# Optimization experiments

Measured on AMD Instinct MI355X. Metric: run time of the kernel, lower is better.

The kernel has to match this reference:

```python
import jax, jax.numpy as jnp
import numpy as np

B, T, D, H = 2, 2048, 2048, 16
HD = D // H
EPS = 1e-8
NEG = -1e9


def setup_inputs() -> dict:
    key = jax.random.key(0)
    ks = jax.random.split(key, 6)
    x = jax.random.normal(ks[0], (B, T, D), dtype=jnp.float32)
    # additive causal mask, broadcast over [B, H, T, T]
    causal = jnp.tril(jnp.ones((T, T), dtype=bool))
    attn_mask = jnp.where(causal, 0.0, NEG).astype(jnp.float32)[None, None]
    s = 1.0 / np.sqrt(D)
    w_norm = jnp.ones((D,), dtype=jnp.float32)
    wq = jax.random.normal(ks[1], (D, D), dtype=jnp.float32) * s
    wk = jax.random.normal(ks[2], (D, D), dtype=jnp.float32) * s
    wv = jax.random.normal(ks[3], (D, D), dtype=jnp.float32) * s
    wo = jax.random.normal(ks[4], (D, D), dtype=jnp.float32) * s
    return {"x": x, "attn_mask": attn_mask, "w_norm": w_norm,
            "wq": wq, "wk": wk, "wv": wv, "wo": wo}


def _rmsnorm(x, w):
    # norm = ||x||_2 * D^-0.5 ; out = w * x / (norm + eps)  (eps outside, as in source)
    norm = jnp.sqrt(jnp.sum(x * x, axis=-1, keepdims=True)) * (x.shape[-1] ** -0.5)
    return w * x / (norm + EPS)


def reference(x, attn_mask, w_norm, wq, wk, wv, wo):
    b, t, d = x.shape
    xn = _rmsnorm(x, w_norm)
    # Linear (no bias): y = x @ W^T ; split into heads -> [B, H, T, HD]
    def proj(w):
        return jnp.einsum('btd,ed->bte', xn, w).reshape(b, t, H, HD).transpose(0, 2, 1, 3)
    q, k, v = proj(wq), proj(wk), proj(wv)
    scale = HD ** -0.5
    w_scores = jnp.einsum('bhqd,bhkd->bhqk', q, k) * scale + attn_mask
    p = jax.nn.softmax(w_scores, axis=-1)
    out = jnp.einsum('bhqk,bhkd->bhqd', p, v)
    out = out.transpose(0, 2, 1, 3).reshape(b, t, d)
    return jnp.einsum('btd,ed->bte', out, wo)
```

## Files before the change

### kernel.cpp

```cpp
#include <hip/hip_runtime.h>
#include <stdint.h>

#define TT 2048
#define DD 2048
#define NHH 16
#define HDD 128
#define BTT 4096

typedef __attribute__((ext_vector_type(8))) short bf16x8;
typedef __attribute__((ext_vector_type(4))) float f32x4;

__device__ __forceinline__ unsigned short f2bf(float f) {
    union { float f; uint32_t u; } v; v.f = f;
    uint32_t u = v.u;
    u += 0x7fffu + ((u >> 16) & 1u);
    return (unsigned short)(u >> 16);
}

__device__ __forceinline__ void gld16(const unsigned short* g, unsigned short* l) {
    __builtin_amdgcn_global_load_lds(
        (const __attribute__((address_space(1))) unsigned int*)g,
        (__attribute__((address_space(3))) unsigned int*)l, 16, 0, 0);
}

__global__ __launch_bounds__(256) void convert_w(const float* __restrict__ wq,
                                                 const float* __restrict__ wk,
                                                 const float* __restrict__ wv,
                                                 const float* __restrict__ wo,
                                                 unsigned short* __restrict__ out) {
    size_t gid = (size_t)blockIdx.x * 256 + threadIdx.x;
    size_t base = gid * 8;
    int which = (int)(base >> 22);
    const float* src = which == 0 ? wq : which == 1 ? wk : which == 2 ? wv : wo;
    size_t off = base & 4194303u;
    float4 a = ((const float4*)(src + off))[0];
    float4 b = ((const float4*)(src + off))[1];
    union { unsigned short us[8]; uint4 v; } pk;
    pk.us[0] = f2bf(a.x); pk.us[1] = f2bf(a.y); pk.us[2] = f2bf(a.z); pk.us[3] = f2bf(a.w);
    pk.us[4] = f2bf(b.x); pk.us[5] = f2bf(b.y); pk.us[6] = f2bf(b.z); pk.us[7] = f2bf(b.w);
    *(uint4*)(out + base) = pk.v;
}

__global__ __launch_bounds__(256) void rmsnorm_k(const float* __restrict__ x,
                                                 const float* __restrict__ w,
                                                 unsigned short* __restrict__ xn) {
    const int row = blockIdx.x;
    const int tid = threadIdx.x;
    const float* xr = x + (size_t)row * DD;
    float4 a = ((const float4*)xr)[tid * 2];
    float4 b = ((const float4*)xr)[tid * 2 + 1];
    float ss = a.x*a.x + a.y*a.y + a.z*a.z + a.w*a.w
             + b.x*b.x + b.y*b.y + b.z*b.z + b.w*b.w;
    #pragma unroll
    for (int m = 1; m < 64; m <<= 1) ss += __shfl_xor(ss, m, 64);
    __shared__ float wss[4];
    if ((tid & 63) == 0) wss[tid >> 6] = ss;
    __syncthreads();
    float total = wss[0] + wss[1] + wss[2] + wss[3];
    float norm = sqrtf(total) * 0.022097086912079612f;
    float inv = 1.0f / (norm + 1e-8f);
    float4 wa = ((const float4*)w)[tid * 2];
    float4 wb = ((const float4*)w)[tid * 2 + 1];
    union { unsigned short us[8]; uint4 v; } pk;
    pk.us[0] = f2bf(wa.x * a.x * inv); pk.us[1] = f2bf(wa.y * a.y * inv);
    pk.us[2] = f2bf(wa.z * a.z * inv); pk.us[3] = f2bf(wa.w * a.w * inv);
    pk.us[4] = f2bf(wb.x * b.x * inv); pk.us[5] = f2bf(wb.y * b.y * inv);
    pk.us[6] = f2bf(wb.z * b.z * inv); pk.us[7] = f2bf(wb.w * b.w * inv);
    ((uint4*)(xn + (size_t)row * DD))[tid] = pk.v;
}

__device__ __forceinline__ void gemm_core(const unsigned short* __restrict__ Ag0,
                                          const unsigned short* __restrict__ Bg0,
                                          unsigned short* As, unsigned short* Bs,
                                          int tid, f32x4 acc[4][4]) {
    const int w = tid >> 6, lane = tid & 63;
    const int l15 = lane & 15, lq = lane >> 4;
    const int wr = (w >> 1) * 64, wc = (w & 1) * 64;
    const unsigned short* ag = Ag0 + (size_t)(w * 16 + (lane >> 2)) * DD + (lane & 3) * 8;
    const unsigned short* bg = Bg0 + (size_t)(w * 16 + (lane >> 2)) * DD + (lane & 3) * 8;
    unsigned short* al = As + w * 512;
    unsigned short* bl = Bs + w * 512;
    for (int k0 = 0; k0 < DD; k0 += 32) {
        __syncthreads();
        gld16(ag + k0, al);
        gld16(ag + k0 + (size_t)64 * DD, al + 64 * 32);
        gld16(bg + k0, bl);
        gld16(bg + k0 + (size_t)64 * DD, bl + 64 * 32);
        __syncthreads();
        bf16x8 af[4], bfr[4];
        #pragma unroll
        for (int i = 0; i < 4; i++)
            af[i] = *(const bf16x8*)(As + (wr + i * 16 + l15) * 32 + lq * 8);
        #pragma unroll
        for (int j = 0; j < 4; j++)
            bfr[j] = *(const bf16x8*)(Bs + (wc + j * 16 + l15) * 32 + lq * 8);
        #pragma unroll
        for (int i = 0; i < 4; i++)
            #pragma unroll
            for (int j = 0; j < 4; j++)
                acc[i][j] = __builtin_amdgcn_mfma_f32_16x16x32_bf16(af[i], bfr[j], acc[i][j], 0, 0, 0);
    }
}

__global__ __launch_bounds__(256) void gemm_qkv(const unsigned short* __restrict__ A,
                                                const unsigned short* __restrict__ W3,
                                                unsigned short* __restrict__ O3) {
    __shared__ __align__(16) unsigned short As[128 * 32];
    __shared__ __align__(16) unsigned short Bs[128 * 32];
    const int tid = threadIdx.x;
    const int wave = tid >> 6, lane = tid & 63;
    const int l15 = lane & 15, lq = lane >> 4;
    const int by = blockIdx.y;
    const int which = by >> 4;
    const unsigned short* Bw = W3 + (size_t)which * DD * DD;
    unsigned short* C = O3 + (size_t)which * BTT * DD;
    const int m0 = blockIdx.x * 128, n0 = (by & 15) * 128;
    const int wr = (wave >> 1) * 64, wc = (wave & 1) * 64;
    const f32x4 zf = {0.f, 0.f, 0.f, 0.f};
    f32x4 acc[4][4];
    #pragma unroll
    for (int i = 0; i < 4; i++)
        #pragma unroll
        for (int j = 0; j < 4; j++) acc[i][j] = zf;
    gemm_core(A + (size_t)m0 * DD, Bw + (size_t)n0 * DD, As, Bs, tid, acc);
    #pragma unroll
    for (int i = 0; i < 4; i++) {
        const int row = m0 + wr + i * 16 + lq * 4;
        #pragma unroll
        for (int j = 0; j < 4; j++) {
            const int col = n0 + wc + j * 16 + l15;
            #pragma unroll
            for (int r = 0; r < 4; r++)
                C[(size_t)(row + r) * DD + col] = f2bf(acc[i][j][r]);
        }
    }
}

__global__ __launch_bounds__(256) void gemm_out(const unsigned short* __restrict__ A,
                                                const unsigned short* __restrict__ Bw,
                                                float* __restrict__ C) {
    __shared__ __align__(16) unsigned short As[128 * 32];
    __shared__ __align__(16) unsigned short Bs[128 * 32];
    const int tid = threadIdx.x;
    const int wave = tid >> 6, lane = tid & 63;
    const int l15 = lane & 15, lq = lane >> 4;
    const int m0 = blockIdx.x * 128, n0 = blockIdx.y * 128;
    const int wr = (wave >> 1) * 64, wc = (wave & 1) * 64;
    const f32x4 zf = {0.f, 0.f, 0.f, 0.f};
    f32x4 acc[4][4];
    #pragma unroll
    for (int i = 0; i < 4; i++)
        #pragma unroll
        for (int j = 0; j < 4; j++) acc[i][j] = zf;
    gemm_core(A + (size_t)m0 * DD, Bw + (size_t)n0 * DD, As, Bs, tid, acc);
    #pragma unroll
    for (int i = 0; i < 4; i++) {
        const int row = m0 + wr + i * 16 + lq * 4;
        #pragma unroll
        for (int j = 0; j < 4; j++) {
            const int col = n0 + wc + j * 16 + l15;
            #pragma unroll
            for (int r = 0; r < 4; r++)
                C[(size_t)(row + r) * DD + col] = acc[i][j][r];
        }
    }
}

__global__ __launch_bounds__(256) void attn_fused(const unsigned short* __restrict__ q,
                                                  const unsigned short* __restrict__ k,
                                                  const unsigned short* __restrict__ v,
                                                  unsigned short* __restrict__ o) {
    constexpr int LKK = 136;
    constexpr int LPP = 72;
    __shared__ __align__(16) unsigned short Ks[64 * LKK];
    __shared__ __align__(16) unsigned short Vts[128 * 64];
    __shared__ __align__(16) unsigned short Ps[4 * 16 * LPP];
    const int h = blockIdx.y, b = blockIdx.z;
    const int tid = threadIdx.x, wave = tid >> 6, lane = tid & 63;
    const int l15 = lane & 15, lq = lane >> 4;
    const size_t rowbase = (size_t)b * TT;
    const int hcol = h * HDD;
    const float scale = 0.08838834764831845f;
    unsigned short* Pw = Ps + wave * 16 * LPP;
    const f32x4 zf = {0.f, 0.f, 0.f, 0.f};

    for (int half = 0; half < 2; half++) {
        const int qj = (half == 0) ? blockIdx.x : 31 - blockIdx.x;
        const int qt0 = qj * 64;
        bf16x8 aq[4];
        {
            const unsigned short* qrp = q + (rowbase + qt0 + wave * 16 + l15) * DD + hcol;
            #pragma unroll
            for (int kk = 0; kk < 4; kk++)
                aq[kk] = *(const bf16x8*)(qrp + kk * 32 + lq * 8);
        }
        f32x4 acc_o[8];
        #pragma unroll
        for (int jh = 0; jh < 8; jh++) acc_o[jh] = zf;
        float m_i[4], l_i[4];
        #pragma unroll
        for (int r = 0; r < 4; r++) { m_i[r] = -1e30f; l_i[r] = 0.f; }
        const int qp0 = qt0 + wave * 16 + lq * 4;
        const int nkt = qj + 1;
        for (int kt = 0; kt < nkt; kt++) {
            __syncthreads();
            {
                const unsigned short* kg = k + (rowbase + kt * 64) * DD + hcol;
                const unsigned short* vg = v + (rowbase + kt * 64) * DD + hcol;
                #pragma unroll
                for (int it = 0; it < 4; it++) {
                    const int idx = it * 2048 + tid * 8;
                    const int rr = idx >> 7, c = idx & 127;
                    *(uint4*)(&Ks[rr * LKK + c]) = *(const uint4*)(kg + (size_t)rr * DD + c);
                    uint4 dv = *(const uint4*)(vg + (size_t)rr * DD + c);
                    const unsigned short* ds = (const unsigned short*)&dv;
                    const int rs = rr ^ (((c >> 3) & 7) << 3);
                    #pragma unroll
                    for (int jj = 0; jj < 8; jj++)
                        Vts[(c + jj) * 64 + rs] = ds[jj];
                }
            }
            __syncthreads();
            f32x4 accs[4];
            #pragma unroll
            for (int j = 0; j < 4; j++) accs[j] = zf;
            #pragma unroll
            for (int j = 0; j < 4; j++)
                #pragma unroll
                for (int kk = 0; kk < 4; kk++) {
                    bf16x8 bk = *(const bf16x8*)(&Ks[(j * 16 + l15) * LKK + kk * 32 + lq * 8]);
                    accs[j] = __builtin_amdgcn_mfma_f32_16x16x32_bf16(aq[kk], bk, accs[j], 0, 0, 0);
                }
            const int kbase = kt * 64;
            float rowmax[4] = {-1e30f, -1e30f, -1e30f, -1e30f};
            #pragma unroll
            for (int j = 0; j < 4; j++) {
                const int kp = kbase + j * 16 + l15;
                #pragma unroll
                for (int r = 0; r < 4; r++) {
                    float s = accs[j][r] * scale;
                    s = (kp > qp0 + r) ? -1e30f : s;
                    accs[j][r] = s;
                    rowmax[r] = fmaxf(rowmax[r], s);
                }
            }
            #pragma unroll
            for (int r = 0; r < 4; r++) {
                float mx = rowmax[r];
                mx = fmaxf(mx, __shfl_xor(mx, 1, 64));
                mx = fmaxf(mx, __shfl_xor(mx, 2, 64));
                mx = fmaxf(mx, __shfl_xor(mx, 4, 64));
                mx = fmaxf(mx, __shfl_xor(mx, 8, 64));
                float m_new = fmaxf(m_i[r], mx);
                float al = __expf(m_i[r] - m_new);
                m_i[r] = m_new;
                l_i[r] *= al;
                #pragma unroll
                for (int jh = 0; jh < 8; jh++) acc_o[jh][r] *= al;
            }
            float rowsum[4] = {0.f, 0.f, 0.f, 0.f};
            #pragma unroll
            for (int j = 0; j < 4; j++)
                #pragma unroll
                for (int r = 0; r < 4; r++) {
                    float p = __expf(accs[j][r] - m_i[r]);
                    rowsum[r] += p;
                    Pw[(lq * 4 + r) * LPP + j * 16 + l15] = f2bf(p);
                }
            #pragma unroll
            for (int r = 0; r < 4; r++) {
                float s = rowsum[r];
                s += __shfl_xor(s, 1, 64);
                s += __shfl_xor(s, 2, 64);
                s += __shfl_xor(s, 4, 64);
                s += __shfl_xor(s, 8, 64);
                l_i[r] += s;
            }
            bf16x8 ap[2];
            #pragma unroll
            for (int kk = 0; kk < 2; kk++)
                ap[kk] = *(const bf16x8*)(&Pw[l15 * LPP + kk * 32 + lq * 8]);
            #pragma unroll
            for (int jh = 0; jh < 8; jh++) {
                const int hd = jh * 16 + l15;
                const int swz = ((hd >> 3) & 7) << 3;
                #pragma unroll
                for (int kk = 0; kk < 2; kk++) {
                    bf16x8 bv = *(const bf16x8*)(&Vts[hd * 64 + ((kk * 32 + lq * 8) ^ swz)]);
                    acc_o[jh] = __builtin_amdgcn_mfma_f32_16x16x32_bf16(ap[kk], bv, acc_o[jh], 0, 0, 0);
                }
            }
        }
        #pragma unroll
        for (int jh = 0; jh < 8; jh++) {
            const int col = hcol + jh * 16 + l15;
            #pragma unroll
            for (int r = 0; r < 4; r++)
                o[(rowbase + qp0 + r) * DD + col] = f2bf(acc_o[jh][r] * (1.0f / l_i[r]));
        }
    }
}

extern "C" void kernel_launch(void* const* d_in, const int* in_sizes, int n_in,
                              void* d_out, int out_size, void* d_ws, size_t ws_size,
                              hipStream_t stream) {
    const float* x      = (const float*)d_in[0];
    const float* w_norm = (const float*)d_in[2];
    const float* wq     = (const float*)d_in[3];
    const float* wk     = (const float*)d_in[4];
    const float* wv     = (const float*)d_in[5];
    const float* wo     = (const float*)d_in[6];

    unsigned short* wbf = (unsigned short*)d_ws;
    unsigned short* xn  = wbf + (size_t)4 * DD * DD;
    unsigned short* qb  = xn + (size_t)BTT * DD;
    unsigned short* kb  = qb + (size_t)BTT * DD;
    unsigned short* vb  = kb + (size_t)BTT * DD;
    unsigned short* ab  = vb + (size_t)BTT * DD;

    convert_w<<<8192, 256, 0, stream>>>(wq, wk, wv, wo, wbf);
    rmsnorm_k<<<BTT, 256, 0, stream>>>(x, w_norm, xn);
    dim3 gqkv(32, 48);
    gemm_qkv<<<gqkv, 256, 0, stream>>>(xn, wbf, qb);
    dim3 gattn(16, NHH, 2);
    attn_fused<<<gattn, 256, 0, stream>>>(qb, kb, vb, ab);
    dim3 gout(32, 16);
    gemm_out<<<gout, 256, 0, stream>>>(ab, wbf + (size_t)3 * DD * DD, (float*)d_out);
}
```

Measured before the change: 482.6 us.

## Double-buffer K/V tiles in attention with register prefetch and MFMA priority

The attention kernel now keeps two LDS buffers for the K and transposed-V tiles. It loads the next tile's K/V into registers before computing on the current tile, then writes them to the other buffer afterwards, which removes one barrier per iteration and hides global load latency behind the MFMA work. It also raises wave priority around the MFMA sections with s_setprio. In exchange, LDS use roughly doubles and register pressure grows, which could lower occupancy.

```diff
diff --git a/kernel.cpp b/kernel.cpp
--- a/kernel.cpp
+++ b/kernel.cpp
@@ -172,8 +172,8 @@
                                                   unsigned short* __restrict__ o) {
     constexpr int LKK = 136;
     constexpr int LPP = 72;
-    __shared__ __align__(16) unsigned short Ks[64 * LKK];
-    __shared__ __align__(16) unsigned short Vts[128 * 64];
+    __shared__ __align__(16) unsigned short Ks[2][64 * LKK];
+    __shared__ __align__(16) unsigned short Vts[2][128 * 64];
     __shared__ __align__(16) unsigned short Ps[4 * 16 * LPP];
     const int h = blockIdx.y, b = blockIdx.z;
     const int tid = threadIdx.x, wave = tid >> 6, lane = tid & 63;
@@ -184,6 +184,16 @@
     unsigned short* Pw = Ps + wave * 16 * LPP;
     const f32x4 zf = {0.f, 0.f, 0.f, 0.f};
 
+    uint4 kr0, kr1, kr2, kr3, vr0, vr1, vr2, vr3;
+    const int sidx = tid * 8;
+    const int srr = sidx >> 7;
+    const int sc  = sidx & 127;
+    const int swz = ((sc >> 3) & 7) << 3;
+    const int srs0 = (srr +  0) ^ swz;
+    const int srs1 = (srr + 16) ^ swz;
+    const int srs2 = (srr + 32) ^ swz;
+    const int srs3 = (srr + 48) ^ swz;
+
     for (int half = 0; half < 2; half++) {
         const int qj = (half == 0) ? blockIdx.x : 31 - blockIdx.x;
         const int qt0 = qj * 64;
@@ -202,35 +212,69 @@
         for (int r = 0; r < 4; r++) { m_i[r] = -1e30f; l_i[r] = 0.f; }
         const int qp0 = qt0 + wave * 16 + lq * 4;
         const int nkt = qj + 1;
+
+        __syncthreads();
+        {
+            const unsigned short* kg = k + (rowbase + 0) * DD + hcol;
+            const unsigned short* vg = v + (rowbase + 0) * DD + hcol;
+            kr0 = *(const uint4*)(kg + (size_t)(srr +  0) * DD + sc);
+            kr1 = *(const uint4*)(kg + (size_t)(srr + 16) * DD + sc);
+            kr2 = *(const uint4*)(kg + (size_t)(srr + 32) * DD + sc);
+            kr3 = *(const uint4*)(kg + (size_t)(srr + 48) * DD + sc);
+            vr0 = *(const uint4*)(vg + (size_t)(srr +  0) * DD + sc);
+            vr1 = *(const uint4*)(vg + (size_t)(srr + 16) * DD + sc);
+            vr2 = *(const uint4*)(vg + (size_t)(srr + 32) * DD + sc);
+            vr3 = *(const uint4*)(vg + (size_t)(srr + 48) * DD + sc);
+        }
+        {
+            unsigned short* ksb = &Ks[0][0];
+            unsigned short* vtb = &Vts[0][0];
+            *(uint4*)(ksb + (srr +  0) * LKK + sc) = kr0;
+            *(uint4*)(ksb + (srr + 16) * LKK + sc) = kr1;
+            *(uint4*)(ksb + (srr + 32) * LKK + sc) = kr2;
+            *(uint4*)(ksb + (srr + 48) * LKK + sc) = kr3;
+            const unsigned short* d0 = (const unsigned short*)&vr0;
+            const unsigned short* d1 = (const unsigned short*)&vr1;
+            const unsigned short* d2 = (const unsigned short*)&vr2;
+            const unsigned short* d3 = (const unsigned short*)&vr3;
+            #pragma unroll
+            for (int jj = 0; jj < 8; jj++) {
+                vtb[(sc + jj) * 64 + srs0] = d0[jj];
+                vtb[(sc + jj) * 64 + srs1] = d1[jj];
+                vtb[(sc + jj) * 64 + srs2] = d2[jj];
+                vtb[(sc + jj) * 64 + srs3] = d3[jj];
+            }
+        }
+
         for (int kt = 0; kt < nkt; kt++) {
+            const int cur = kt & 1;
+            if (kt + 1 < nkt) {
+                const unsigned short* kg = k + (rowbase + (kt + 1) * 64) * DD + hcol;
+                const unsigned short* vg = v + (rowbase + (kt + 1) * 64) * DD + hcol;
+                kr0 = *(const uint4*)(kg + (size_t)(srr +  0) * DD + sc);
+                kr1 = *(const uint4*)(kg + (size_t)(srr + 16) * DD + sc);
+                kr2 = *(const uint4*)(kg + (size_t)(srr + 32) * DD + sc);
+                kr3 = *(const uint4*)(kg + (size_t)(srr + 48) * DD + sc);
+                vr0 = *(const uint4*)(vg + (size_t)(srr +  0) * DD + sc);
+                vr1 = *(const uint4*)(vg + (size_t)(srr + 16) * DD + sc);
+                vr2 = *(const uint4*)(vg + (size_t)(srr + 32) * DD + sc);
+                vr3 = *(const uint4*)(vg + (size_t)(srr + 48) * DD + sc);
+            }
             __syncthreads();
-            {
-                const unsigned short* kg = k + (rowbase + kt * 64) * DD + hcol;
-                const unsigned short* vg = v + (rowbase + kt * 64) * DD + hcol;
-                #pragma unroll
-                for (int it = 0; it < 4; it++) {
-                    const int idx = it * 2048 + tid * 8;
-                    const int rr = idx >> 7, c = idx & 127;
-                    *(uint4*)(&Ks[rr * LKK + c]) = *(const uint4*)(kg + (size_t)rr * DD + c);
-                    uint4 dv = *(const uint4*)(vg + (size_t)rr * DD + c);
-                    const unsigned short* ds = (const unsigned short*)&dv;
-                    const int rs = rr ^ (((c >> 3) & 7) << 3);
-                    #pragma unroll
-                    for (int jj = 0; jj < 8; jj++)
-                        Vts[(c + jj) * 64 + rs] = ds[jj];
-                }
-            }
-            __syncthreads();
+            const unsigned short* ksc = &Ks[cur][0];
+            const unsigned short* vtc = &Vts[cur][0];
             f32x4 accs[4];
             #pragma unroll
             for (int j = 0; j < 4; j++) accs[j] = zf;
+            __builtin_amdgcn_s_setprio(1);
             #pragma unroll
             for (int j = 0; j < 4; j++)
                 #pragma unroll
                 for (int kk = 0; kk < 4; kk++) {
-                    bf16x8 bk = *(const bf16x8*)(&Ks[(j * 16 + l15) * LKK + kk * 32 + lq * 8]);
+                    bf16x8 bk = *(const bf16x8*)(&ksc[(j * 16 + l15) * LKK + kk * 32 + lq * 8]);
                     accs[j] = __builtin_amdgcn_mfma_f32_16x16x32_bf16(aq[kk], bk, accs[j], 0, 0, 0);
                 }
+            __builtin_amdgcn_s_setprio(0);
             const int kbase = kt * 64;
             float rowmax[4] = {-1e30f, -1e30f, -1e30f, -1e30f};
             #pragma unroll
@@ -280,14 +324,35 @@
             #pragma unroll
             for (int kk = 0; kk < 2; kk++)
                 ap[kk] = *(const bf16x8*)(&Pw[l15 * LPP + kk * 32 + lq * 8]);
+            __builtin_amdgcn_s_setprio(1);
             #pragma unroll
             for (int jh = 0; jh < 8; jh++) {
                 const int hd = jh * 16 + l15;
-                const int swz = ((hd >> 3) & 7) << 3;
+                const int vswz = ((hd >> 3) & 7) << 3;
                 #pragma unroll
                 for (int kk = 0; kk < 2; kk++) {
-                    bf16x8 bv = *(const bf16x8*)(&Vts[hd * 64 + ((kk * 32 + lq * 8) ^ swz)]);
+                    bf16x8 bv = *(const bf16x8*)(&vtc[hd * 64 + ((kk * 32 + lq * 8) ^ vswz)]);
                     acc_o[jh] = __builtin_amdgcn_mfma_f32_16x16x32_bf16(ap[kk], bv, acc_o[jh], 0, 0, 0);
+                }
+            }
+            __builtin_amdgcn_s_setprio(0);
+            if (kt + 1 < nkt) {
+                unsigned short* ksb = &Ks[cur ^ 1][0];
+                unsigned short* vtb = &Vts[cur ^ 1][0];
+                *(uint4*)(ksb + (srr +  0) * LKK + sc) = kr0;
+                *(uint4*)(ksb + (srr + 16) * LKK + sc) = kr1;
+                *(uint4*)(ksb + (srr + 32) * LKK + sc) = kr2;
+                *(uint4*)(ksb + (srr + 48) * LKK + sc) = kr3;
+                const unsigned short* d0 = (const unsigned short*)&vr0;
+                const unsigned short* d1 = (const unsigned short*)&vr1;
+                const unsigned short* d2 = (const unsigned short*)&vr2;
+                const unsigned short* d3 = (const unsigned short*)&vr3;
+                #pragma unroll
+                for (int jj = 0; jj < 8; jj++) {
+                    vtb[(sc + jj) * 64 + srs0] = d0[jj];
+                    vtb[(sc + jj) * 64 + srs1] = d1[jj];
+                    vtb[(sc + jj) * 64 + srs2] = d2[jj];
+                    vtb[(sc + jj) * 64 + srs3] = d3[jj];
                 }
             }
         }
```

Result: slower. 501.4 us (+3.9%).
